# Kernel optimization log

Hardware: AMD Instinct MI355X
Metric: run time of the kernel (lower is better)

The kernel has to match this reference:

```python
import jax, jax.numpy as jnp
import numpy as np

N = 20000      # nodes
E = 320000     # edges
IN = 128       # in_channels
HID = 64       # hidden_channels (per-head out dim, concat=False -> mean over heads)
HEADS = 4
NEG_SLOPE = 0.2


def setup_inputs() -> dict:
    key = jax.random.key(0)
    ks = jax.random.split(key, 18)
    g = lambda i, shape: jax.random.normal(ks[i], shape, dtype=jnp.float32) * 0.05
    return {
        "x": jax.random.normal(ks[0], (N, IN), dtype=jnp.float32),
        "edge_index": jax.random.randint(ks[1], (2, E), 0, N),
        # GATConv params: lin weight (no bias in PyG lin), att_src/att_dst, out bias
        "W0": g(2, (IN, HEADS * HID)),
        "W1": g(3, (HID, HEADS * HID)),
        "W2": g(4, (HID, HEADS * HID)),
        "W3": g(5, (HID, HEADS * HID)),
        "a_src": g(6, (4, HEADS, HID)),
        "a_dst": g(7, (4, HEADS, HID)),
        "gat_b": g(8, (4, HID)),
        # residual projection for layer 0 (in_channels != hidden_channels)
        "res_W": g(9, (IN, HID)),
        "res_b": g(10, (HID,)),
        # edge classifier MLP: 2*HID -> HID -> HID -> 1
        "lin_W0": g(11, (2 * HID, HID)),
        "lin_b0": g(12, (HID,)),
        "lin_W1": g(13, (HID, HID)),
        "lin_b1": g(14, (HID,)),
        "lin_W2": g(15, (HID, 1)),
        "lin_b2": g(16, (1,)),
    }


def gat_conv(x, src, dst, W, asrc, adst, b, n):
    # x: [n, F_in]; src/dst: [E_tot] (self-loops included); W: [F_in, H*C]
    h = (x @ W).reshape(n, HEADS, HID)                     # [n, H, C]
    s_src = (h * asrc).sum(-1)                             # [n, H]
    s_dst = (h * adst).sum(-1)                             # [n, H]
    e = jax.nn.leaky_relu(s_src[src] + s_dst[dst], NEG_SLOPE)  # [E_tot, H]
    # segment softmax over incoming edges of each dst node
    m = jax.ops.segment_max(e, dst, num_segments=n)        # [n, H]
    p = jnp.exp(e - m[dst])
    z = jax.ops.segment_sum(p, dst, num_segments=n)
    alpha = p / z[dst]                                     # [E_tot, H]
    out = jax.ops.segment_sum(alpha[:, :, None] * h[src], dst, num_segments=n)  # [n, H, C]
    return out.mean(axis=1) + b                            # concat=False -> mean over heads


def reference(x, edge_index, W0, W1, W2, W3, a_src, a_dst, gat_b,
              res_W, res_b, lin_W0, lin_b0, lin_W1, lin_b1, lin_W2, lin_b2):
    n = x.shape[0]
    loop = jnp.arange(n)
    src = jnp.concatenate([edge_index[0], loop])  # PyG GATConv adds self-loops
    dst = jnp.concatenate([edge_index[1], loop])
    Ws = [W0, W1, W2, W3]
    h = x
    for i in range(4):
        h_prev = h
        h = gat_conv(h, src, dst, Ws[i], a_src[i], a_dst[i], gat_b[i], n)
        if i == 0:
            h = h + h_prev @ res_W + res_b   # projected residual
        else:
            h = h + h_prev
        h = jax.nn.elu(h)
    row, col = edge_index[0], edge_index[1]
    er = jnp.concatenate([h[row], h[col]], axis=1)        # [E, 2*HID]
    er = jax.nn.relu(er @ lin_W0 + lin_b0)                # shapes differ -> no residual
    er = jax.nn.relu(er @ lin_W1 + lin_b1 + er)           # shapes match -> residual
    logits = er @ lin_W2 + lin_b2                          # [E, 1]
    return logits
```

## Files before the change

kernel.cpp:

```cpp
#include <hip/hip_runtime.h>
#include <hip/hip_bf16.h>

#define NSLOPE 0.2f

typedef short bf16x8 __attribute__((ext_vector_type(8)));
typedef float f32x4 __attribute__((ext_vector_type(4)));

__device__ __forceinline__ unsigned short f2b(float f) {
    unsigned u = __float_as_uint(f);
    unsigned r = (u + 0x7FFFu + ((u >> 16) & 1u)) >> 16;
    return (unsigned short)r;
}
__device__ __forceinline__ float b2f_lo(unsigned w) {
    return __uint_as_float(w << 16);
}
__device__ __forceinline__ float b2f_hi(unsigned w) {
    return __uint_as_float(w & 0xFFFF0000u);
}
__device__ __forceinline__ float b2f_s(short s) {
    return __uint_as_float(((unsigned)(unsigned short)s) << 16);
}


__global__ __launch_bounds__(256) void hist_deg(const int* __restrict__ ei,
                                                int* __restrict__ deg, int E,
                                                int n) {
    int t = blockIdx.x * 256 + threadIdx.x;
    int Etot = E + n;
    if (t >= Etot) return;
    int d = (t < E) ? ei[E + t] : (t - E);
    atomicAdd(&deg[d], 1);
}

__global__ __launch_bounds__(256) void scan_blk(const int* __restrict__ deg,
                                                int* __restrict__ local,
                                                int* __restrict__ bsum, int n) {
    __shared__ int sm[256];
    const int base = blockIdx.x * 1024;
    const int t = threadIdx.x;
    const int i0 = base + t * 4;
    int v0 = 0, v1 = 0, v2 = 0, v3 = 0;
    if (i0 + 3 < n) {
        int4 v = *(const int4*)(deg + i0);
        v0 = v.x; v1 = v.y; v2 = v.z; v3 = v.w;
    } else {
        if (i0 < n) v0 = deg[i0];
        if (i0 + 1 < n) v1 = deg[i0 + 1];
        if (i0 + 2 < n) v2 = deg[i0 + 2];
    }
    int s = v0 + v1 + v2 + v3;
    sm[t] = s;
    __syncthreads();
    for (int off = 1; off < 256; off <<= 1) {
        int val = (t >= off) ? sm[t - off] : 0;
        __syncthreads();
        sm[t] += val;
        __syncthreads();
    }
    int ex = sm[t] - s;
    if (t == 255) bsum[blockIdx.x] = sm[255];
    if (i0 < n) local[i0] = ex;
    if (i0 + 1 < n) local[i0 + 1] = ex + v0;
    if (i0 + 2 < n) local[i0 + 2] = ex + v0 + v1;
    if (i0 + 3 < n) local[i0 + 3] = ex + v0 + v1 + v2;
}

__global__ __launch_bounds__(256) void scan_top(const int* __restrict__ bsum,
                                                int* __restrict__ boff,
                                                int nb) {
    __shared__ int sm[256];
    const int t = threadIdx.x;
    int s = (t < nb) ? bsum[t] : 0;
    sm[t] = s;
    __syncthreads();
    for (int off = 1; off < 256; off <<= 1) {
        int val = (t >= off) ? sm[t - off] : 0;
        __syncthreads();
        sm[t] += val;
        __syncthreads();
    }
    if (t < nb) boff[t] = sm[t] - s;
}

__global__ __launch_bounds__(256) void scan_add(const int* __restrict__ local,
                                                const int* __restrict__ boff,
                                                int* __restrict__ rowstart,
                                                int* __restrict__ cursor,
                                                int n, int Etot) {
    int i = blockIdx.x * 256 + threadIdx.x;
    if (i > n) return;
    if (i == n) {
        rowstart[n] = Etot;
        return;
    }
    int v = local[i] + boff[i >> 10];
    rowstart[i] = v;
    cursor[i] = v;
}

__global__ __launch_bounds__(256) void fill_csr(const int* __restrict__ ei,
                                                int* __restrict__ cursor,
                                                int2* __restrict__ csr2, int E,
                                                int n) {
    int t = blockIdx.x * 256 + threadIdx.x;
    int Etot = E + n;
    if (t >= Etot) return;
    int s, d;
    if (t < E) { s = ei[t]; d = ei[E + t]; } else { s = d = t - E; }
    int pos = atomicAdd(&cursor[d], 1);
    csr2[pos] = make_int2(s, d);
}

__global__ __launch_bounds__(256) void prep_weights(
    const float* __restrict__ W0, const float* __restrict__ W1,
    const float* __restrict__ W2, const float* __restrict__ W3,
    const float* __restrict__ resW, const float* __restrict__ linW0,
    const float* __restrict__ linW1, const float* __restrict__ linB0,
    short* __restrict__ Wt0, short* __restrict__ Wt1, short* __restrict__ Wt2,
    short* __restrict__ Wt3, short* __restrict__ WtR, short* __restrict__ WtU,
    short* __restrict__ WtV, short* __restrict__ WbT,
    float* __restrict__ bias128) {
    const float* src;
    short* dst;
    int K, NC, rowoff = 0;
    switch (blockIdx.x) {
        case 0: src = W0; dst = Wt0; K = 128; NC = 256; break;
        case 1: src = W1; dst = Wt1; K = 64; NC = 256; break;
        case 2: src = W2; dst = Wt2; K = 64; NC = 256; break;
        case 3: src = W3; dst = Wt3; K = 64; NC = 256; break;
        case 4: src = resW; dst = WtR; K = 128; NC = 64; break;
        case 5: src = linW0; dst = WtU; K = 64; NC = 64; break;
        case 6: src = linW0; dst = WtV; K = 64; NC = 64; rowoff = 64; break;
        case 7: src = linW1; dst = WbT; K = 64; NC = 64; break;
        default: {
            if (blockIdx.y == 0 && threadIdx.x < 128)
                bias128[threadIdx.x] =
                    (threadIdx.x < 64) ? linB0[threadIdx.x] : 0.f;
            return;
        }
    }
    for (int idx = blockIdx.y * 256 + threadIdx.x; idx < K * NC;
         idx += 256 * 16) {
        int k = idx / NC, nn = idx - k * NC;
        dst[nn * K + k] = (short)f2b(src[(k + rowoff) * NC + nn]);
    }
}

__global__ __launch_bounds__(256) void convert_x(const float* __restrict__ x,
                                                 short* __restrict__ xb,
                                                 int total) {
    int idx = (blockIdx.x * 256 + threadIdx.x) * 4;
    if (idx >= total) return;
    float4 v = *(const float4*)(x + idx);
    ushort4 o;
    o.x = f2b(v.x); o.y = f2b(v.y); o.z = f2b(v.z); o.w = f2b(v.w);
    *(ushort4*)(xb + idx) = o;
}

template <int K, int NG, int OM>
__global__ __launch_bounds__(256) void mfma_gemm(
    const short* __restrict__ Xb, const short* __restrict__ Wt,
    const float* __restrict__ bias, uint2* __restrict__ Hq,
    const float* __restrict__ as_l, const float* __restrict__ ad_l,
    float* __restrict__ Ssrc, float* __restrict__ Sdst,
    float* __restrict__ OutF, short* __restrict__ OutB, int n) {
    constexpr int XSTR = K + 8;
    constexpr int NC = NG * 16;
    __shared__ __align__(16) short Xs[64 * XSTR];
    __shared__ __align__(16) short Ws[NC * 40];
    const int tid = threadIdx.x;
    const int nb = blockIdx.x * 64;
    constexpr int CH = K / 8;
    for (int idx = tid; idx < 64 * CH; idx += 256) {
        int row = idx / CH, c = idx - row * CH;
        uint4 v = make_uint4(0, 0, 0, 0);
        if (nb + row < n)
            v = *(const uint4*)(Xb + (size_t)(nb + row) * K + c * 8);
        *(uint4*)(Xs + row * XSTR + c * 8) = v;
    }
    const int wid = tid >> 6;
    const int lane = tid & 63;
    const int t = lane & 15, quad = lane >> 4;
    f32x4 acc[NG];
#pragma unroll
    for (int g = 0; g < NG; ++g) acc[g] = (f32x4){0.f, 0.f, 0.f, 0.f};
#pragma unroll 1
    for (int kc = 0; kc < K / 32; ++kc) {
        __syncthreads();
        for (int idx = tid; idx < NC * 4; idx += 256) {
            int row = idx >> 2, c = idx & 3;
            uint4 v = *(const uint4*)(Wt + (size_t)row * K + kc * 32 + c * 8);
            *(uint4*)(Ws + row * 40 + c * 8) = v;
        }
        __syncthreads();
        bf16x8 a =
            *(const bf16x8*)(Xs + (wid * 16 + t) * XSTR + kc * 32 + quad * 8);
#pragma unroll
        for (int g = 0; g < NG; ++g) {
            bf16x8 b = *(const bf16x8*)(Ws + (g * 16 + t) * 40 + quad * 8);
            acc[g] = __builtin_amdgcn_mfma_f32_16x16x32_bf16(a, b, acc[g], 0, 0, 0);
        }
    }
    if (OM == 1) {
#pragma unroll
        for (int r = 0; r < 4; ++r) {
            int node = nb + wid * 16 + quad * 4 + r;
            if (node >= n) continue;
#pragma unroll
            for (int g = 0; g < 4; ++g) {
                unsigned p01 = ((unsigned)f2b(acc[g + 4][r]) << 16) |
                               (unsigned)f2b(acc[g][r]);
                unsigned p23 = ((unsigned)f2b(acc[g + 12][r]) << 16) |
                               (unsigned)f2b(acc[g + 8][r]);
                Hq[(size_t)node * 64 + g * 16 + t] = make_uint2(p01, p23);
            }
        }
        float asv[16], adv[16];
#pragma unroll
        for (int G = 0; G < 16; ++G) {
            asv[G] = as_l[G * 16 + t];
            adv[G] = ad_l[G * 16 + t];
        }
#pragma unroll
        for (int r = 0; r < 4; ++r) {
            int node = nb + wid * 16 + quad * 4 + r;
            float pv[8];
#pragma unroll
            for (int h = 0; h < 4; ++h) {
                float ps = 0.f, pd = 0.f;
#pragma unroll
                for (int j = 0; j < 4; ++j) {
                    float a = acc[h * 4 + j][r];
                    ps += a * asv[h * 4 + j];
                    pd += a * adv[h * 4 + j];
                }
                pv[h] = ps;
                pv[4 + h] = pd;
            }
#pragma unroll
            for (int off = 1; off < 16; off <<= 1) {
#pragma unroll
                for (int i = 0; i < 8; ++i) pv[i] += __shfl_xor(pv[i], off, 64);
            }
            if (t == 0 && node < n) {
                *(float4*)&Ssrc[node * 4] =
                    make_float4(pv[0], pv[1], pv[2], pv[3]);
                *(float4*)&Sdst[node * 4] =
                    make_float4(pv[4], pv[5], pv[6], pv[7]);
            }
        }
    } else {
        float bv[NG];
#pragma unroll
        for (int g = 0; g < NG; ++g) bv[g] = bias ? bias[g * 16 + t] : 0.f;
#pragma unroll
        for (int r = 0; r < 4; ++r) {
            int node = nb + wid * 16 + quad * 4 + r;
            if (node >= n) continue;
            if (OM == 0) {
#pragma unroll
                for (int g = 0; g < NG; ++g)
                    OutF[(size_t)node * NC + g * 16 + t] = acc[g][r] + bv[g];
            } else {
#pragma unroll
                for (int g = 0; g < NG; ++g)
                    OutB[(size_t)node * NC + g * 16 + t] =
                        (short)f2b(acc[g][r] + bv[g]);
            }
        }
    }
}

__global__ __launch_bounds__(256) void edge_scores(
    const int2* __restrict__ csr2, const float* __restrict__ Ssrc,
    const float* __restrict__ Sdst, float4* __restrict__ p4, int Etot) {
    int e = blockIdx.x * 256 + threadIdx.x;
    if (e >= Etot) return;
    int2 sd = csr2[e];
    float4 ss = *(const float4*)&Ssrc[sd.x * 4];
    float4 dd = *(const float4*)&Sdst[sd.y * 4];
    float c0 = ss.x + dd.x, c1 = ss.y + dd.y, c2 = ss.z + dd.z,
          c3 = ss.w + dd.w;
    c0 = c0 > 0.f ? c0 : NSLOPE * c0;
    c1 = c1 > 0.f ? c1 : NSLOPE * c1;
    c2 = c2 > 0.f ? c2 : NSLOPE * c2;
    c3 = c3 > 0.f ? c3 : NSLOPE * c3;
    p4[e] = make_float4(__expf(c0), __expf(c1), __expf(c2), __expf(c3));
}

__global__ __launch_bounds__(256) void gat_gather(
    const int2* __restrict__ csr2, const int* __restrict__ rowstart,
    const float4* __restrict__ p4, const uint2* __restrict__ Hq,
    const float* __restrict__ gb, const float* __restrict__ resid,
    float* __restrict__ featOut, short* __restrict__ featB, int n) {
    const int wid = threadIdx.x >> 6;
    const int lane = threadIdx.x & 63;
    const int node = blockIdx.x * 4 + wid;
    if (node >= n) return;
    const int start = __builtin_amdgcn_readfirstlane(rowstart[node]);
    const int end = __builtin_amdgcn_readfirstlane(rowstart[node + 1]);
    float u0 = 0.f, u1 = 0.f, u2 = 0.f, u3 = 0.f;
    float z0 = 0.f, z1 = 0.f, z2 = 0.f, z3 = 0.f;
#pragma unroll 4
    for (int e = start; e < end; ++e) {
        int sj = csr2[e].x;
        float4 p = p4[e];
        uint2 hv = Hq[(size_t)sj * 64 + lane];
        u0 += p.x * b2f_lo(hv.x);
        u1 += p.y * b2f_hi(hv.x);
        u2 += p.z * b2f_lo(hv.y);
        u3 += p.w * b2f_hi(hv.y);
        z0 += p.x; z1 += p.y; z2 += p.z; z3 += p.w;
    }
    float val = 0.25f * (u0 / z0 + u1 / z1 + u2 / z2 + u3 / z3) + gb[lane] +
                resid[(size_t)node * 64 + lane];
    val = val > 0.f ? val : expm1f(val);
    featOut[(size_t)node * 64 + lane] = val;
    featB[(size_t)node * 64 + lane] = (short)f2b(val);
}

__global__ __launch_bounds__(256) void edge_mlp3(
    const int* __restrict__ ei, const unsigned* __restrict__ UV,
    const short* __restrict__ WbT, const float* __restrict__ bb,
    const float* __restrict__ Wc, const float* __restrict__ bc,
    float* __restrict__ out, int E) {
    __shared__ __align__(16) short t1b[64 * 72];
    __shared__ __align__(16) short wbs[64 * 72];
    const int tid = threadIdx.x;
    const int eBase = blockIdx.x * 64;
    for (int idx = tid; idx < 512; idx += 256) {
        int row = idx >> 3, c = idx & 7;
        *(uint4*)(wbs + row * 72 + c * 8) =
            *(const uint4*)(WbT + row * 64 + c * 8);
    }
    {
        const int j = tid & 31;
        const int eg = tid >> 5;
        int rr[8], cc[8];
#pragma unroll
        for (int it = 0; it < 8; ++it) {
            int e = eBase + it * 8 + eg;
            rr[it] = (e < E) ? ei[e] : 0;
            cc[it] = (e < E) ? ei[E + e] : 0;
        }
#pragma unroll
        for (int it = 0; it < 8; ++it) {
            unsigned uu = UV[(size_t)rr[it] * 64 + j];
            unsigned vv = UV[(size_t)cc[it] * 64 + 32 + j];
            float lo = fmaxf(b2f_lo(uu) + b2f_lo(vv), 0.f);
            float hi = fmaxf(b2f_hi(uu) + b2f_hi(vv), 0.f);
            *(unsigned*)(t1b + (it * 8 + eg) * 72 + j * 2) =
                ((unsigned)f2b(hi) << 16) | (unsigned)f2b(lo);
        }
    }
    __syncthreads();
    const int w = tid >> 6, lane = tid & 63;
    const int t = lane & 15, quad = lane >> 4;
    f32x4 acc[4];
#pragma unroll
    for (int g = 0; g < 4; ++g) acc[g] = (f32x4){0.f, 0.f, 0.f, 0.f};
#pragma unroll
    for (int kc = 0; kc < 2; ++kc) {
        bf16x8 a = *(const bf16x8*)(t1b + (w * 16 + t) * 72 + kc * 32 + quad * 8);
#pragma unroll
        for (int g = 0; g < 4; ++g) {
            bf16x8 b = *(const bf16x8*)(wbs + (g * 16 + t) * 72 + kc * 32 + quad * 8);
            acc[g] = __builtin_amdgcn_mfma_f32_16x16x32_bf16(a, b, acc[g], 0, 0, 0);
        }
    }
    float wcv[4], bbv[4];
#pragma unroll
    for (int g = 0; g < 4; ++g) {
        wcv[g] = Wc[g * 16 + t];
        bbv[g] = bb[g * 16 + t];
    }
    const float bcv = bc[0];
#pragma unroll
    for (int r = 0; r < 4; ++r) {
        int el = w * 16 + quad * 4 + r;
        float part = 0.f;
#pragma unroll
        for (int g = 0; g < 4; ++g) {
            float t1v = b2f_s(t1b[el * 72 + g * 16 + t]);
            float t2 = fmaxf(acc[g][r] + bbv[g] + t1v, 0.f);
            part += t2 * wcv[g];
        }
        part += __shfl_xor(part, 1, 64);
        part += __shfl_xor(part, 2, 64);
        part += __shfl_xor(part, 4, 64);
        part += __shfl_xor(part, 8, 64);
        int e = eBase + el;
        if (t == 0 && e < E) out[e] = part + bcv;
    }
}

extern "C" void kernel_launch(void* const* d_in, const int* in_sizes, int n_in,
                              void* d_out, int out_size, void* d_ws,
                              size_t ws_size, hipStream_t stream) {
    const float* x = (const float*)d_in[0];
    const int* ei = (const int*)d_in[1];
    const float* W0 = (const float*)d_in[2];
    const float* W1 = (const float*)d_in[3];
    const float* W2 = (const float*)d_in[4];
    const float* W3 = (const float*)d_in[5];
    const float* a_src = (const float*)d_in[6];
    const float* a_dst = (const float*)d_in[7];
    const float* gat_b = (const float*)d_in[8];
    const float* res_W = (const float*)d_in[9];
    const float* res_b = (const float*)d_in[10];
    const float* lin_W0 = (const float*)d_in[11];
    const float* lin_b0 = (const float*)d_in[12];
    const float* lin_W1 = (const float*)d_in[13];
    const float* lin_b1 = (const float*)d_in[14];
    const float* lin_W2 = (const float*)d_in[15];
    const float* lin_b2 = (const float*)d_in[16];
    float* out = (float*)d_out;

    const int N = in_sizes[0] / 128;
    const int E = in_sizes[1] / 2;
    const int Etot = E + N;

    float* ws = (float*)d_ws;
    uint2* Hq = (uint2*)ws;
    float* feat = (float*)(Hq + (size_t)N * 64);
    float* res = feat + (size_t)N * 64;
    short* xb = (short*)(res + (size_t)N * 64);
    short* featb = xb;
    float* Ssrc = (float*)(xb + (size_t)N * 128);
    float* Sdst = Ssrc + (size_t)N * 4;
    short* Wt0 = (short*)(Sdst + (size_t)N * 4);
    short* Wt1 = Wt0 + 256 * 128;
    short* Wt2 = Wt1 + 256 * 64;
    short* Wt3 = Wt2 + 256 * 64;
    short* WtR = Wt3 + 256 * 64;
    short* WtU = WtR + 64 * 128;
    short* WtV = WtU + 64 * 64;
    short* WbT = WtV + 64 * 64;
    int* deg = (int*)(WbT + 64 * 64);
    int* rowstart = deg + N;
    int* cursor = rowstart + N + 1;
    int* locals = cursor + N;
    int* bsum = locals + N;
    int* boff = bsum + 256;
    float* bias128 = (float*)(boff + 256);
    int2* csr2 = (int2*)(((size_t)(bias128 + 128) + 15) & ~(size_t)15);
    float4* p4 = (float4*)(((size_t)(csr2 + Etot) + 15) & ~(size_t)15);
    short* UVb = (short*)Hq;

    const int gemmBlocks = (N + 63) / 64;
    const int edgeBlocks = (Etot + 255) / 256;
    const int nodeW = (N + 3) / 4;
    const int scanBlocks = (N + 1023) / 1024;
    const short* Wts[4] = {Wt0, Wt1, Wt2, Wt3};

    hipMemsetAsync(deg, 0, (size_t)N * sizeof(int), stream);
    hist_deg<<<edgeBlocks, 256, 0, stream>>>(ei, deg, E, N);
    scan_blk<<<scanBlocks, 256, 0, stream>>>(deg, locals, bsum, N);
    scan_top<<<1, 256, 0, stream>>>(bsum, boff, scanBlocks);
    scan_add<<<(N + 256) / 256, 256, 0, stream>>>(locals, boff, rowstart,
                                                  cursor, N, Etot);
    fill_csr<<<edgeBlocks, 256, 0, stream>>>(ei, cursor, csr2, E, N);

    prep_weights<<<dim3(9, 16), 256, 0, stream>>>(
        W0, W1, W2, W3, res_W, lin_W0, lin_W1, lin_b0, Wt0, Wt1, Wt2, Wt3,
        WtR, WtU, WtV, WbT, bias128);
    convert_x<<<(N * 128 / 4 + 255) / 256, 256, 0, stream>>>(x, xb, N * 128);

    for (int i = 0; i < 4; ++i) {
        if (i == 0)
            mfma_gemm<128, 16, 1><<<gemmBlocks, 256, 0, stream>>>(
                xb, Wt0, nullptr, Hq, a_src, a_dst, Ssrc, Sdst, nullptr,
                nullptr, N);
        else
            mfma_gemm<64, 16, 1><<<gemmBlocks, 256, 0, stream>>>(
                featb, Wts[i], nullptr, Hq, a_src + i * 256, a_dst + i * 256,
                Ssrc, Sdst, nullptr, nullptr, N);
        edge_scores<<<edgeBlocks, 256, 0, stream>>>(csr2, Ssrc, Sdst, p4,
                                                    Etot);
        if (i == 0)
            mfma_gemm<128, 4, 0><<<gemmBlocks, 256, 0, stream>>>(
                xb, WtR, res_b, nullptr, nullptr, nullptr, nullptr, nullptr,
                res, nullptr, N);
        const float* resid = (i == 0) ? res : feat;
        gat_gather<<<nodeW, 256, 0, stream>>>(csr2, rowstart, p4, Hq,
                                              gat_b + i * 64, resid, feat,
                                              featb, N);
    }

    mfma_gemm<64, 8, 2><<<gemmBlocks, 256, 0, stream>>>(
        featb, WtU, bias128, nullptr, nullptr, nullptr, nullptr, nullptr,
        nullptr, UVb, N);
    edge_mlp3<<<(E + 63) / 64, 256, 0, stream>>>(
        ei, (const unsigned*)UVb, WbT, lin_b1, lin_W2, lin_b2, out, E);
}
```

Baseline: 353.3 us.

## Aggregate features before projection in GAT layers and fuse epilogue into GEMM

Reorders each GAT layer to gather-and-softmax-weight the narrower input features per head, then apply W via an MFMA GEMM over the concatenated per-head aggregates. Attention scores are computed from precomputed W·a vectors, applied to the input features inside the conversion kernel or the previous layer's GEMM epilogue. Bias, residual and ELU move into the GEMM epilogue. This cuts the bytes gathered per edge in later layers, at the cost of writing and reading a wider per-node aggregate buffer and a larger-K GEMM.

```diff
diff --git a/kernel.cpp b/kernel.cpp
--- a/kernel.cpp
+++ b/kernel.cpp
@@ -19,6 +19,9 @@
 }
 __device__ __forceinline__ float b2f_s(short s) {
     return __uint_as_float(((unsigned)(unsigned short)s) << 16);
+}
+__device__ __forceinline__ unsigned packb(float lo, float hi) {
+    return ((unsigned)f2b(hi) << 16) | (unsigned)f2b(lo);
 }
 
 
@@ -116,18 +119,29 @@
     const float* __restrict__ W2, const float* __restrict__ W3,
     const float* __restrict__ resW, const float* __restrict__ linW0,
     const float* __restrict__ linW1, const float* __restrict__ linB0,
-    short* __restrict__ Wt0, short* __restrict__ Wt1, short* __restrict__ Wt2,
-    short* __restrict__ Wt3, short* __restrict__ WtR, short* __restrict__ WtU,
-    short* __restrict__ WtV, short* __restrict__ WbT,
-    float* __restrict__ bias128) {
+    short* __restrict__ WtC0, short* __restrict__ WtC1,
+    short* __restrict__ WtC2, short* __restrict__ WtC3,
+    short* __restrict__ WtR, short* __restrict__ WtU, short* __restrict__ WtV,
+    short* __restrict__ WbT, float* __restrict__ bias128) {
+    const int bx = blockIdx.x;
+    if (bx < 4) {
+        const float* src = (bx == 0) ? W0 : (bx == 1) ? W1 : (bx == 2) ? W2 : W3;
+        short* dst = (bx == 0) ? WtC0 : (bx == 1) ? WtC1 : (bx == 2) ? WtC2 : WtC3;
+        const int K = (bx == 0) ? 128 : 64;
+        const int total = 64 * 4 * K;
+        for (int idx = blockIdx.y * 256 + threadIdx.x; idx < total;
+             idx += 256 * 16) {
+            int j = idx / (4 * K);
+            int rem = idx - j * 4 * K;
+            int h = rem / K, k = rem - h * K;
+            dst[idx] = (short)f2b(src[k * 256 + h * 64 + j]);
+        }
+        return;
+    }
     const float* src;
     short* dst;
     int K, NC, rowoff = 0;
-    switch (blockIdx.x) {
-        case 0: src = W0; dst = Wt0; K = 128; NC = 256; break;
-        case 1: src = W1; dst = Wt1; K = 64; NC = 256; break;
-        case 2: src = W2; dst = Wt2; K = 64; NC = 256; break;
-        case 3: src = W3; dst = Wt3; K = 64; NC = 256; break;
+    switch (bx) {
         case 4: src = resW; dst = WtR; K = 128; NC = 64; break;
         case 5: src = linW0; dst = WtU; K = 64; NC = 64; break;
         case 6: src = linW0; dst = WtV; K = 64; NC = 64; rowoff = 64; break;
@@ -146,24 +160,57 @@
     }
 }
 
-__global__ __launch_bounds__(256) void convert_x(const float* __restrict__ x,
-                                                 short* __restrict__ xb,
-                                                 int total) {
-    int idx = (blockIdx.x * 256 + threadIdx.x) * 4;
-    if (idx >= total) return;
-    float4 v = *(const float4*)(x + idx);
-    ushort4 o;
-    o.x = f2b(v.x); o.y = f2b(v.y); o.z = f2b(v.z); o.w = f2b(v.w);
-    *(ushort4*)(xb + idx) = o;
+__global__ __launch_bounds__(256) void prep_wsd(
+    const float* __restrict__ W0, const float* __restrict__ W1,
+    const float* __restrict__ W2, const float* __restrict__ W3,
+    const float* __restrict__ a_src, const float* __restrict__ a_dst,
+    float* __restrict__ wsd0, float* __restrict__ wsdL) {
+    const int l = blockIdx.x;
+    const float* W = (l == 0) ? W0 : (l == 1) ? W1 : (l == 2) ? W2 : W3;
+    const int K = (l == 0) ? 128 : 64;
+    float* dst = (l == 0) ? wsd0 : wsdL + (l - 1) * 64 * 8;
+    for (int idx = threadIdx.x; idx < K * 8; idx += 256) {
+        int k = idx >> 3, j = idx & 7, h = j & 3;
+        const float* av = ((j < 4) ? a_src : a_dst) + l * 256 + h * 64;
+        const float* wr = W + k * 256 + h * 64;
+        float s = 0.f;
+#pragma unroll 8
+        for (int c = 0; c < 64; ++c) s += wr[c] * av[c];
+        dst[k * 8 + j] = s;
+    }
+}
+
+__global__ __launch_bounds__(256) void convert_x_scores(
+    const float* __restrict__ x, const float* __restrict__ wsd0,
+    unsigned* __restrict__ xb2, float* __restrict__ Ssrc,
+    float* __restrict__ Sdst, int n) {
+    const int wid = threadIdx.x >> 6;
+    const int lane = threadIdx.x & 63;
+    const int node = blockIdx.x * 4 + wid;
+    if (node >= n) return;
+    float2 xv = *(const float2*)&x[(size_t)node * 128 + lane * 2];
+    xb2[(size_t)node * 64 + lane] = packb(xv.x, xv.y);
+    float pv[8];
+    const float* w0 = &wsd0[(lane * 2) * 8];
+    const float* w1 = &wsd0[(lane * 2 + 1) * 8];
+#pragma unroll
+    for (int j = 0; j < 8; ++j) pv[j] = xv.x * w0[j] + xv.y * w1[j];
+#pragma unroll
+    for (int off = 1; off < 64; off <<= 1) {
+#pragma unroll
+        for (int j = 0; j < 8; ++j) pv[j] += __shfl_xor(pv[j], off, 64);
+    }
+    if (lane == 0) {
+        *(float4*)&Ssrc[node * 4] = make_float4(pv[0], pv[1], pv[2], pv[3]);
+        *(float4*)&Sdst[node * 4] = make_float4(pv[4], pv[5], pv[6], pv[7]);
+    }
 }
 
 template <int K, int NG, int OM>
 __global__ __launch_bounds__(256) void mfma_gemm(
     const short* __restrict__ Xb, const short* __restrict__ Wt,
-    const float* __restrict__ bias, uint2* __restrict__ Hq,
-    const float* __restrict__ as_l, const float* __restrict__ ad_l,
-    float* __restrict__ Ssrc, float* __restrict__ Sdst,
-    float* __restrict__ OutF, short* __restrict__ OutB, int n) {
+    const float* __restrict__ bias, float* __restrict__ OutF,
+    short* __restrict__ OutB, int n) {
     constexpr int XSTR = K + 8;
     constexpr int NC = NG * 16;
     __shared__ __align__(16) short Xs[64 * XSTR];
@@ -201,71 +248,121 @@
             acc[g] = __builtin_amdgcn_mfma_f32_16x16x32_bf16(a, b, acc[g], 0, 0, 0);
         }
     }
-    if (OM == 1) {
-#pragma unroll
-        for (int r = 0; r < 4; ++r) {
-            int node = nb + wid * 16 + quad * 4 + r;
-            if (node >= n) continue;
+    float bv[NG];
+#pragma unroll
+    for (int g = 0; g < NG; ++g) bv[g] = bias ? bias[g * 16 + t] : 0.f;
+#pragma unroll
+    for (int r = 0; r < 4; ++r) {
+        int node = nb + wid * 16 + quad * 4 + r;
+        if (node >= n) continue;
+        if (OM == 0) {
+#pragma unroll
+            for (int g = 0; g < NG; ++g)
+                OutF[(size_t)node * NC + g * 16 + t] = acc[g][r] + bv[g];
+        } else {
+#pragma unroll
+            for (int g = 0; g < NG; ++g)
+                OutB[(size_t)node * NC + g * 16 + t] =
+                    (short)f2b(acc[g][r] + bv[g]);
+        }
+    }
+}
+
+template <int KK, bool SCORES>
+__global__ __launch_bounds__(256) void gemm_layer(
+    const short* __restrict__ Xb, const short* __restrict__ Wt,
+    const float* __restrict__ gbias, const float* __restrict__ resid,
+    const float* __restrict__ wsd, float* __restrict__ feat,
+    short* __restrict__ featb, float* __restrict__ Ssrc,
+    float* __restrict__ Sdst, int n) {
+    __shared__ __align__(16) short Xs[64 * 136];
+    __shared__ __align__(16) short Ws[64 * 40];
+    const int tid = threadIdx.x;
+    const int nb = blockIdx.x * 64;
+    const int wid = tid >> 6;
+    const int lane = tid & 63;
+    const int t = lane & 15, quad = lane >> 4;
+    f32x4 acc[4];
+#pragma unroll
+    for (int g = 0; g < 4; ++g) acc[g] = (f32x4){0.f, 0.f, 0.f, 0.f};
+#pragma unroll 1
+    for (int c0 = 0; c0 < KK / 128; ++c0) {
+        __syncthreads();
+        for (int idx = tid; idx < 1024; idx += 256) {
+            int row = idx >> 4, c = idx & 15;
+            uint4 v = make_uint4(0, 0, 0, 0);
+            if (nb + row < n)
+                v = *(const uint4*)(Xb + (size_t)(nb + row) * KK + c0 * 128 +
+                                    c * 8);
+            *(uint4*)(Xs + row * 136 + c * 8) = v;
+        }
+#pragma unroll 1
+        for (int kc = 0; kc < 4; ++kc) {
+            __syncthreads();
+            for (int idx = tid; idx < 256; idx += 256) {
+                int row = idx >> 2, c = idx & 3;
+                uint4 v = *(const uint4*)(Wt + (size_t)row * KK + c0 * 128 +
+                                          kc * 32 + c * 8);
+                *(uint4*)(Ws + row * 40 + c * 8) = v;
+            }
+            __syncthreads();
+            bf16x8 a =
+                *(const bf16x8*)(Xs + (wid * 16 + t) * 136 + kc * 32 + quad * 8);
 #pragma unroll
             for (int g = 0; g < 4; ++g) {
-                unsigned p01 = ((unsigned)f2b(acc[g + 4][r]) << 16) |
-                               (unsigned)f2b(acc[g][r]);
-                unsigned p23 = ((unsigned)f2b(acc[g + 12][r]) << 16) |
-                               (unsigned)f2b(acc[g + 8][r]);
-                Hq[(size_t)node * 64 + g * 16 + t] = make_uint2(p01, p23);
+                bf16x8 b = *(const bf16x8*)(Ws + (g * 16 + t) * 40 + quad * 8);
+                acc[g] =
+                    __builtin_amdgcn_mfma_f32_16x16x32_bf16(a, b, acc[g], 0, 0, 0);
             }
         }
-        float asv[16], adv[16];
-#pragma unroll
-        for (int G = 0; G < 16; ++G) {
-            asv[G] = as_l[G * 16 + t];
-            adv[G] = ad_l[G * 16 + t];
-        }
-#pragma unroll
-        for (int r = 0; r < 4; ++r) {
-            int node = nb + wid * 16 + quad * 4 + r;
+    }
+    float bv[4];
+#pragma unroll
+    for (int g = 0; g < 4; ++g) bv[g] = gbias[g * 16 + t];
+    float wsv[4][8];
+    if (SCORES) {
+#pragma unroll
+        for (int g = 0; g < 4; ++g) {
+            float4 lo = *(const float4*)&wsd[(g * 16 + t) * 8];
+            float4 hi = *(const float4*)&wsd[(g * 16 + t) * 8 + 4];
+            wsv[g][0] = lo.x; wsv[g][1] = lo.y; wsv[g][2] = lo.z;
+            wsv[g][3] = lo.w; wsv[g][4] = hi.x; wsv[g][5] = hi.y;
+            wsv[g][6] = hi.z; wsv[g][7] = hi.w;
+        }
+    }
+#pragma unroll
+    for (int r = 0; r < 4; ++r) {
+        int node = nb + wid * 16 + quad * 4 + r;
+        bool ok = node < n;
+        float val[4];
+#pragma unroll
+        for (int g = 0; g < 4; ++g) {
+            float v = acc[g][r] + bv[g];
+            if (ok) v += resid[(size_t)node * 64 + g * 16 + t];
+            v = v > 0.f ? v : expm1f(v);
+            val[g] = v;
+            if (ok) {
+                feat[(size_t)node * 64 + g * 16 + t] = v;
+                featb[(size_t)node * 64 + g * 16 + t] = (short)f2b(v);
+            }
+        }
+        if (SCORES) {
             float pv[8];
 #pragma unroll
-            for (int h = 0; h < 4; ++h) {
-                float ps = 0.f, pd = 0.f;
-#pragma unroll
-                for (int j = 0; j < 4; ++j) {
-                    float a = acc[h * 4 + j][r];
-                    ps += a * asv[h * 4 + j];
-                    pd += a * adv[h * 4 + j];
-                }
-                pv[h] = ps;
-                pv[4 + h] = pd;
+            for (int j = 0; j < 8; ++j) {
+                pv[j] = val[0] * wsv[0][j] + val[1] * wsv[1][j] +
+                        val[2] * wsv[2][j] + val[3] * wsv[3][j];
             }
 #pragma unroll
             for (int off = 1; off < 16; off <<= 1) {
 #pragma unroll
-                for (int i = 0; i < 8; ++i) pv[i] += __shfl_xor(pv[i], off, 64);
+                for (int j = 0; j < 8; ++j) pv[j] += __shfl_xor(pv[j], off, 64);
             }
-            if (t == 0 && node < n) {
+            if (t == 0 && ok) {
                 *(float4*)&Ssrc[node * 4] =
                     make_float4(pv[0], pv[1], pv[2], pv[3]);
                 *(float4*)&Sdst[node * 4] =
                     make_float4(pv[4], pv[5], pv[6], pv[7]);
-            }
-        }
-    } else {
-        float bv[NG];
-#pragma unroll
-        for (int g = 0; g < NG; ++g) bv[g] = bias ? bias[g * 16 + t] : 0.f;
-#pragma unroll
-        for (int r = 0; r < 4; ++r) {
-            int node = nb + wid * 16 + quad * 4 + r;
-            if (node >= n) continue;
-            if (OM == 0) {
-#pragma unroll
-                for (int g = 0; g < NG; ++g)
-                    OutF[(size_t)node * NC + g * 16 + t] = acc[g][r] + bv[g];
-            } else {
-#pragma unroll
-                for (int g = 0; g < NG; ++g)
-                    OutB[(size_t)node * NC + g * 16 + t] =
-                        (short)f2b(acc[g][r] + bv[g]);
             }
         }
     }
@@ -288,35 +385,81 @@
     p4[e] = make_float4(__expf(c0), __expf(c1), __expf(c2), __expf(c3));
 }
 
-__global__ __launch_bounds__(256) void gat_gather(
+__global__ __launch_bounds__(256) void gat_gather128(
     const int2* __restrict__ csr2, const int* __restrict__ rowstart,
-    const float4* __restrict__ p4, const uint2* __restrict__ Hq,
-    const float* __restrict__ gb, const float* __restrict__ resid,
-    float* __restrict__ featOut, short* __restrict__ featB, int n) {
+    const float4* __restrict__ p4, const unsigned* __restrict__ xin,
+    unsigned* __restrict__ aggB, int n) {
     const int wid = threadIdx.x >> 6;
     const int lane = threadIdx.x & 63;
     const int node = blockIdx.x * 4 + wid;
     if (node >= n) return;
-    const int start = __builtin_amdgcn_readfirstlane(rowstart[node]);
-    const int end = __builtin_amdgcn_readfirstlane(rowstart[node + 1]);
-    float u0 = 0.f, u1 = 0.f, u2 = 0.f, u3 = 0.f;
+    const int start = rowstart[node];
+    const int end = rowstart[node + 1];
+    float u00 = 0.f, u01 = 0.f, u10 = 0.f, u11 = 0.f;
+    float u20 = 0.f, u21 = 0.f, u30 = 0.f, u31 = 0.f;
     float z0 = 0.f, z1 = 0.f, z2 = 0.f, z3 = 0.f;
 #pragma unroll 4
     for (int e = start; e < end; ++e) {
         int sj = csr2[e].x;
         float4 p = p4[e];
-        uint2 hv = Hq[(size_t)sj * 64 + lane];
-        u0 += p.x * b2f_lo(hv.x);
-        u1 += p.y * b2f_hi(hv.x);
-        u2 += p.z * b2f_lo(hv.y);
-        u3 += p.w * b2f_hi(hv.y);
+        unsigned fv = xin[(size_t)sj * 64 + lane];
+        float f0 = b2f_lo(fv), f1 = b2f_hi(fv);
+        u00 += p.x * f0; u01 += p.x * f1;
+        u10 += p.y * f0; u11 += p.y * f1;
+        u20 += p.z * f0; u21 += p.z * f1;
+        u30 += p.w * f0; u31 += p.w * f1;
         z0 += p.x; z1 += p.y; z2 += p.z; z3 += p.w;
     }
-    float val = 0.25f * (u0 / z0 + u1 / z1 + u2 / z2 + u3 / z3) + gb[lane] +
-                resid[(size_t)node * 64 + lane];
-    val = val > 0.f ? val : expm1f(val);
-    featOut[(size_t)node * 64 + lane] = val;
-    featB[(size_t)node * 64 + lane] = (short)f2b(val);
+    float i0 = 0.25f / z0, i1 = 0.25f / z1, i2 = 0.25f / z2, i3 = 0.25f / z3;
+    size_t base = (size_t)node * 256;
+    aggB[base + lane] = packb(u00 * i0, u01 * i0);
+    aggB[base + 64 + lane] = packb(u10 * i1, u11 * i1);
+    aggB[base + 128 + lane] = packb(u20 * i2, u21 * i2);
+    aggB[base + 192 + lane] = packb(u30 * i3, u31 * i3);
+}
+
+__global__ __launch_bounds__(256) void gat_gather64(
+    const int2* __restrict__ csr2, const int* __restrict__ rowstart,
+    const float4* __restrict__ p4, const unsigned* __restrict__ fin,
+    unsigned* __restrict__ aggB, int n) {
+    const int wid = threadIdx.x >> 6;
+    const int lane = threadIdx.x & 63;
+    const int half = lane >> 5;
+    const int cl = lane & 31;
+    const int node = blockIdx.x * 4 + wid;
+    if (node >= n) return;
+    const int start = rowstart[node];
+    const int end = rowstart[node + 1];
+    float u00 = 0.f, u01 = 0.f, u10 = 0.f, u11 = 0.f;
+    float u20 = 0.f, u21 = 0.f, u30 = 0.f, u31 = 0.f;
+    float z0 = 0.f, z1 = 0.f, z2 = 0.f, z3 = 0.f;
+#pragma unroll 4
+    for (int e = start + half; e < end; e += 2) {
+        int sj = csr2[e].x;
+        float4 p = p4[e];
+        unsigned fv = fin[(size_t)sj * 32 + cl];
+        float f0 = b2f_lo(fv), f1 = b2f_hi(fv);
+        u00 += p.x * f0; u01 += p.x * f1;
+        u10 += p.y * f0; u11 += p.y * f1;
+        u20 += p.z * f0; u21 += p.z * f1;
+        u30 += p.w * f0; u31 += p.w * f1;
+        z0 += p.x; z1 += p.y; z2 += p.z; z3 += p.w;
+    }
+    u00 += __shfl_xor(u00, 32, 64); u01 += __shfl_xor(u01, 32, 64);
+    u10 += __shfl_xor(u10, 32, 64); u11 += __shfl_xor(u11, 32, 64);
+    u20 += __shfl_xor(u20, 32, 64); u21 += __shfl_xor(u21, 32, 64);
+    u30 += __shfl_xor(u30, 32, 64); u31 += __shfl_xor(u31, 32, 64);
+    z0 += __shfl_xor(z0, 32, 64); z1 += __shfl_xor(z1, 32, 64);
+    z2 += __shfl_xor(z2, 32, 64); z3 += __shfl_xor(z3, 32, 64);
+    if (half == 0) {
+        float i0 = 0.25f / z0, i1 = 0.25f / z1, i2 = 0.25f / z2,
+              i3 = 0.25f / z3;
+        size_t base = (size_t)node * 128;
+        aggB[base + cl] = packb(u00 * i0, u01 * i0);
+        aggB[base + 32 + cl] = packb(u10 * i1, u11 * i1);
+        aggB[base + 64 + cl] = packb(u20 * i2, u21 * i2);
+        aggB[base + 96 + cl] = packb(u30 * i3, u31 * i3);
+    }
 }
 
 __global__ __launch_bounds__(256) void edge_mlp3(
@@ -349,8 +492,7 @@
             unsigned vv = UV[(size_t)cc[it] * 64 + 32 + j];
             float lo = fmaxf(b2f_lo(uu) + b2f_lo(vv), 0.f);
             float hi = fmaxf(b2f_hi(uu) + b2f_hi(vv), 0.f);
-            *(unsigned*)(t1b + (it * 8 + eg) * 72 + j * 2) =
-                ((unsigned)f2b(hi) << 16) | (unsigned)f2b(lo);
+            *(unsigned*)(t1b + (it * 8 + eg) * 72 + j * 2) = packb(lo, hi);
         }
     }
     __syncthreads();
@@ -420,38 +562,41 @@
     const int E = in_sizes[1] / 2;
     const int Etot = E + N;
 
-    float* ws = (float*)d_ws;
-    uint2* Hq = (uint2*)ws;
-    float* feat = (float*)(Hq + (size_t)N * 64);
-    float* res = feat + (size_t)N * 64;
+    char* ws = (char*)d_ws;
+    unsigned* aggB = (unsigned*)ws;
+    float* featA = (float*)(aggB + (size_t)N * 256);
+    float* featB = featA + (size_t)N * 64;
+    short* featbA = (short*)(featB + (size_t)N * 64);
+    short* featbB = featbA + (size_t)N * 64;
+    float* res = (float*)(featbB + (size_t)N * 64);
     short* xb = (short*)(res + (size_t)N * 64);
-    short* featb = xb;
     float* Ssrc = (float*)(xb + (size_t)N * 128);
     float* Sdst = Ssrc + (size_t)N * 4;
-    short* Wt0 = (short*)(Sdst + (size_t)N * 4);
-    short* Wt1 = Wt0 + 256 * 128;
-    short* Wt2 = Wt1 + 256 * 64;
-    short* Wt3 = Wt2 + 256 * 64;
-    short* WtR = Wt3 + 256 * 64;
+    short* WtC0 = (short*)(Sdst + (size_t)N * 4);
+    short* WtC1 = WtC0 + 64 * 512;
+    short* WtC2 = WtC1 + 64 * 256;
+    short* WtC3 = WtC2 + 64 * 256;
+    short* WtR = WtC3 + 64 * 256;
     short* WtU = WtR + 64 * 128;
     short* WtV = WtU + 64 * 64;
     short* WbT = WtV + 64 * 64;
-    int* deg = (int*)(WbT + 64 * 64);
+    float* wsd0 = (float*)(WbT + 64 * 64);
+    float* wsdL = wsd0 + 128 * 8;
+    float* bias128 = wsdL + 3 * 64 * 8;
+    int* deg = (int*)(bias128 + 128);
     int* rowstart = deg + N;
     int* cursor = rowstart + N + 1;
     int* locals = cursor + N;
     int* bsum = locals + N;
     int* boff = bsum + 256;
-    float* bias128 = (float*)(boff + 256);
-    int2* csr2 = (int2*)(((size_t)(bias128 + 128) + 15) & ~(size_t)15);
+    int2* csr2 = (int2*)(((size_t)(boff + 256) + 15) & ~(size_t)15);
     float4* p4 = (float4*)(((size_t)(csr2 + Etot) + 15) & ~(size_t)15);
-    short* UVb = (short*)Hq;
+    unsigned* UVb = aggB;
 
     const int gemmBlocks = (N + 63) / 64;
     const int edgeBlocks = (Etot + 255) / 256;
     const int nodeW = (N + 3) / 4;
     const int scanBlocks = (N + 1023) / 1024;
-    const short* Wts[4] = {Wt0, Wt1, Wt2, Wt3};
 
     hipMemsetAsync(deg, 0, (size_t)N * sizeof(int), stream);
     hist_deg<<<edgeBlocks, 256, 0, stream>>>(ei, deg, E, N);
@@ -462,34 +607,39 @@
     fill_csr<<<edgeBlocks, 256, 0, stream>>>(ei, cursor, csr2, E, N);
 
     prep_weights<<<dim3(9, 16), 256, 0, stream>>>(
-        W0, W1, W2, W3, res_W, lin_W0, lin_W1, lin_b0, Wt0, Wt1, Wt2, Wt3,
+        W0, W1, W2, W3, res_W, lin_W0, lin_W1, lin_b0, WtC0, WtC1, WtC2, WtC3,
         WtR, WtU, WtV, WbT, bias128);
-    convert_x<<<(N * 128 / 4 + 255) / 256, 256, 0, stream>>>(x, xb, N * 128);
-
-    for (int i = 0; i < 4; ++i) {
-        if (i == 0)
-            mfma_gemm<128, 16, 1><<<gemmBlocks, 256, 0, stream>>>(
-                xb, Wt0, nullptr, Hq, a_src, a_dst, Ssrc, Sdst, nullptr,
-                nullptr, N);
+    prep_wsd<<<4, 256, 0, stream>>>(W0, W1, W2, W3, a_src, a_dst, wsd0, wsdL);
+    convert_x_scores<<<nodeW, 256, 0, stream>>>(x, wsd0, (unsigned*)xb, Ssrc,
+                                                Sdst, N);
+    mfma_gemm<128, 4, 0><<<gemmBlocks, 256, 0, stream>>>(xb, WtR, res_b, res,
+                                                         nullptr, N);
+
+    edge_scores<<<edgeBlocks, 256, 0, stream>>>(csr2, Ssrc, Sdst, p4, Etot);
+    gat_gather128<<<nodeW, 256, 0, stream>>>(csr2, rowstart, p4,
+                                             (const unsigned*)xb, aggB, N);
+    gemm_layer<512, true><<<gemmBlocks, 256, 0, stream>>>(
+        (const short*)aggB, WtC0, gat_b, res, wsdL, featA, featbA, Ssrc, Sdst,
+        N);
+    const short* WtCs[3] = {WtC1, WtC2, WtC3};
+    float* feats[4] = {featA, featB, featA, featB};
+    short* featbs[4] = {featbA, featbB, featbA, featbB};
+    for (int i = 1; i < 4; ++i) {
+        edge_scores<<<edgeBlocks, 256, 0, stream>>>(csr2, Ssrc, Sdst, p4, Etot);
+        gat_gather64<<<nodeW, 256, 0, stream>>>(
+            csr2, rowstart, p4, (const unsigned*)featbs[i - 1], aggB, N);
+        if (i < 3)
+            gemm_layer<256, true><<<gemmBlocks, 256, 0, stream>>>(
+                (const short*)aggB, WtCs[i - 1], gat_b + i * 64, feats[i - 1],
+                wsdL + i * 64 * 8, feats[i], featbs[i], Ssrc, Sdst, N);
         else
-            mfma_gemm<64, 16, 1><<<gemmBlocks, 256, 0, stream>>>(
-                featb, Wts[i], nullptr, Hq, a_src + i * 256, a_dst + i * 256,
-                Ssrc, Sdst, nullptr, nullptr, N);
-        edge_scores<<<edgeBlocks, 256, 0, stream>>>(csr2, Ssrc, Sdst, p4,
-                                                    Etot);
-        if (i == 0)
-            mfma_gemm<128, 4, 0><<<gemmBlocks, 256, 0, stream>>>(
-                xb, WtR, res_b, nullptr, nullptr, nullptr, nullptr, nullptr,
-                res, nullptr, N);
-        const float* resid = (i == 0) ? res : feat;
-        gat_gather<<<nodeW, 256, 0, stream>>>(csr2, rowstart, p4, Hq,
-                                              gat_b + i * 64, resid, feat,
-                                              featb, N);
+            gemm_layer<256, false><<<gemmBlocks, 256, 0, stream>>>(
+                (const short*)aggB, WtCs[i - 1], gat_b + i * 64, feats[i - 1],
+                nullptr, feats[i], featbs[i], Ssrc, Sdst, N);
     }
 
     mfma_gemm<64, 8, 2><<<gemmBlocks, 256, 0, stream>>>(
-        featb, WtU, bias128, nullptr, nullptr, nullptr, nullptr, nullptr,
-        nullptr, UVb, N);
-    edge_mlp3<<<(E + 63) / 64, 256, 0, stream>>>(
-        ei, (const unsigned*)UVb, WbT, lin_b1, lin_W2, lin_b2, out, E);
-}
+        featbB, WtU, bias128, nullptr, (short*)UVb, N);
+    edge_mlp3<<<(E + 63) / 64, 256, 0, stream>>>(ei, UVb, WbT, lin_b1, lin_W2,
+                                                 lin_b2, out, E);
+}
```

Result: no change. 353.7 us (+0.1%).
